# Performance work log

Hardware: AMD Instinct MI355X
Metric: run time of the kernel (lower is better)

## Reference

```python
import jax, jax.numpy as jnp
import numpy as np

B, H, G, EPG = 32768, 4096, 16, 16
E = G * EPG  # 256 total experts
STD = 0.02


def setup_inputs() -> dict:
    key = jax.random.key(0)
    k1, k2, k3 = jax.random.split(key, 3)
    hidden_states = jax.random.normal(k1, (B, H), dtype=jnp.float32)
    group_w = STD * jax.random.normal(k2, (G, H), dtype=jnp.float32)   # group_router.weight
    expert_w = STD * jax.random.normal(k3, (G, EPG, H), dtype=jnp.float32)  # stacked expert_routers[g].weight
    return {"hidden_states": hidden_states, "group_w": group_w, "expert_w": expert_w}


def reference(hidden_states, group_w, expert_w):
    b, h = hidden_states.shape
    g, epg, _ = expert_w.shape
    e = g * epg

    # Level 1: group routing (argmax of softmax == argmax of logits)
    group_logits = hidden_states @ group_w.T                      # [B, G]
    selected_groups = jnp.argmax(group_logits, axis=-1)           # [B]

    # Level 2: expert logits for every group, then gather the selected group's block.
    # (Math identical to per-token loop computing only the selected group's router.)
    logits_all = jnp.einsum('bh,geh->bge', hidden_states, expert_w)  # [B, G, EPG]
    sel_logits = jnp.take_along_axis(
        logits_all, selected_groups[:, None, None], axis=1)[:, 0, :]  # [B, EPG]

    expert_probs = jax.nn.softmax(sel_logits, axis=-1)            # [B, EPG]
    local_idx = jnp.argmax(expert_probs, axis=-1)                 # [B]
    selected_experts = selected_groups * epg + local_idx          # [B]
    expert_weights = jnp.take_along_axis(expert_probs, local_idx[:, None], axis=1)[:, 0]  # [B]

    # Scatter the selected group's logits into the global [B, E] tensor (rest zero).
    rows = jnp.arange(b)[:, None]                                 # [B, 1]
    cols = selected_groups[:, None] * epg + jnp.arange(epg)[None, :]  # [B, EPG]
    all_expert_logits = jnp.zeros((b, e), dtype=hidden_states.dtype).at[rows, cols].set(sel_logits)

    return all_expert_logits, selected_experts[:, None], expert_weights[:, None]
```

## Files before the change

### kernel.cpp

```cpp
#include <hip/hip_runtime.h>


constexpr int Btok = 32768;
constexpr int Hdim = 4096;
constexpr int Gn   = 16;
constexpr int EPGn = 16;
constexpr int En   = 256;
constexpr int Hq   = Hdim / 4;
constexpr int TILE = 1024;

__global__ __launch_bounds__(256) void k_group(
    const float* __restrict__ hidden, const float* __restrict__ gw,
    unsigned char* __restrict__ gsel)
{
  const int lane = threadIdx.x & 63;
  const int wq = __builtin_amdgcn_readfirstlane((int)(threadIdx.x >> 6));
  const int token = blockIdx.x * 64 + lane;
  const float* hrow  = hidden + (size_t)token * Hdim + wq * Hq;
  const float* wbase = gw + wq * Hq;

  float acc[Gn];
#pragma unroll
  for (int g = 0; g < Gn; ++g) acc[g] = 0.f;

#pragma unroll 2
  for (int j = 0; j < Hq; j += 4) {
    const float4 h4 = *reinterpret_cast<const float4*>(hrow + j);
#pragma unroll
    for (int g = 0; g < Gn; ++g) {
      const float* wg = wbase + g * Hdim + j;
      acc[g] += h4.x * wg[0] + h4.y * wg[1] + h4.z * wg[2] + h4.w * wg[3];
    }
  }

  __shared__ float part[4][64][Gn + 1];
#pragma unroll
  for (int g = 0; g < Gn; ++g) part[wq][lane][g] = acc[g];
  __syncthreads();

  if (wq == 0) {
    float best = -3.4e38f; int bi = 0;
#pragma unroll
    for (int g = 0; g < Gn; ++g) {
      float v = part[0][lane][g] + part[1][lane][g]
              + part[2][lane][g] + part[3][lane][g];
      if (v > best) { best = v; bi = g; }
    }
    gsel[token] = (unsigned char)bi;
  }
}

__global__ __launch_bounds__(256) void k_expert(
    const float* __restrict__ hidden, const float* __restrict__ ew,
    const unsigned char* __restrict__ gsel,
    float* __restrict__ out0,
    float* __restrict__ out1,
    float* __restrict__ out2)
{
  const int g = blockIdx.x;
  const int tbase = blockIdx.y * TILE;

  __shared__ int   list[TILE];
  __shared__ int   cnt;
  __shared__ float part[4][64][EPGn + 1];
  __shared__ float lrow[64][EPGn + 1];

  if (threadIdx.x == 0) cnt = 0;
  __syncthreads();
  for (int i = threadIdx.x; i < TILE; i += 256) {
    if ((int)gsel[tbase + i] == g) {
      int p = atomicAdd(&cnt, 1);
      list[p] = tbase + i;
    }
  }
  __syncthreads();
  const int n = cnt;

  const int lane = threadIdx.x & 63;
  const int wq = __builtin_amdgcn_readfirstlane((int)(threadIdx.x >> 6));
  const float* wbase = ew + ((size_t)g * EPGn) * Hdim + wq * Hq;

  for (int s0 = 0; s0 < n; s0 += 64) {
    const int ns = min(64, n - s0);
    const int token = list[s0 + ((lane < ns) ? lane : 0)];
    const float* hrow = hidden + (size_t)token * Hdim + wq * Hq;

    float acc[EPGn];
#pragma unroll
    for (int e = 0; e < EPGn; ++e) acc[e] = 0.f;

#pragma unroll 2
    for (int j = 0; j < Hq; j += 4) {
      const float4 h4 = *reinterpret_cast<const float4*>(hrow + j);
#pragma unroll
      for (int e = 0; e < EPGn; ++e) {
        const float* we = wbase + e * Hdim + j;
        acc[e] += h4.x * we[0] + h4.y * we[1] + h4.z * we[2] + h4.w * we[3];
      }
    }

#pragma unroll
    for (int e = 0; e < EPGn; ++e) part[wq][lane][e] = acc[e];
    __syncthreads();

    if (wq == 0 && lane < ns) {
      float l[EPGn];
      float m = -3.4e38f;
#pragma unroll
      for (int e = 0; e < EPGn; ++e) {
        l[e] = part[0][lane][e] + part[1][lane][e]
             + part[2][lane][e] + part[3][lane][e];
        m = fmaxf(m, l[e]);
      }
      float sum = 0.f;
#pragma unroll
      for (int e = 0; e < EPGn; ++e) sum += expf(l[e] - m);
      int bi = 0; float best = l[0];
#pragma unroll
      for (int e = 1; e < EPGn; ++e) { if (l[e] > best) { best = l[e]; bi = e; } }
      const int tok = list[s0 + lane];
      out1[tok] = (float)(g * EPGn + bi);
      out2[tok] = 1.f / sum;
#pragma unroll
      for (int e = 0; e < EPGn; ++e) lrow[lane][e] = l[e];
    }
    __syncthreads();

    const int r = threadIdx.x >> 2;
    const int p = threadIdx.x & 3;
    if (r < ns) {
      const int tok = list[s0 + r];
      float* row = out0 + (size_t)tok * En;
#pragma unroll
      for (int i = 0; i < 16; ++i) {
        float4 v;
        if (i == g) {
          v.x = lrow[r][p * 4 + 0];
          v.y = lrow[r][p * 4 + 1];
          v.z = lrow[r][p * 4 + 2];
          v.w = lrow[r][p * 4 + 3];
        } else {
          v.x = 0.f; v.y = 0.f; v.z = 0.f; v.w = 0.f;
        }
        *reinterpret_cast<float4*>(row + i * 16 + p * 4) = v;
      }
    }
    __syncthreads();
  }
}

extern "C" void kernel_launch(void* const* d_in, const int* in_sizes, int n_in,
                              void* d_out, int out_size, void* d_ws, size_t ws_size,
                              hipStream_t stream) {
  const float* hidden = (const float*)d_in[0];
  const float* gw     = (const float*)d_in[1];
  const float* ew     = (const float*)d_in[2];
  float* out0 = (float*)d_out;
  unsigned char* gsel = (unsigned char*)d_ws;

  k_group<<<Btok / 64, 256, 0, stream>>>(hidden, gw, gsel);

  float* out1 = out0 + (size_t)Btok * En;
  float* out2 = out1 + Btok;
  k_expert<<<dim3(Gn, Btok / TILE), 256, 0, stream>>>(
      hidden, ew, gsel, out0, out1, out2);
}
```

Measured before the change: 1.270 ms.

## Split hidden dim across 16 waves and parallelize reductions with shuffles

Both kernels move from 256-thread to 1024-thread blocks. The hidden dimension is now split across 16 wavefronts instead of 4, so each wave does a quarter of the dot-product work and occupancy rises. The partial sums are reduced in two LDS stages. Softmax, argmax and group-argmax then run in parallel across 16 lanes per token with xor shuffles, replacing a single wave that looped serially, and each lane writes one 16-wide slice of the output row. The change also uses the fast __expf, picks the lowest index on ties, and sets a launch bound of (1024, 8) that may squeeze register allocation.

```diff
diff --git a/kernel.cpp b/kernel.cpp
--- a/kernel.cpp
+++ b/kernel.cpp
@@ -6,25 +6,26 @@
 constexpr int Gn   = 16;
 constexpr int EPGn = 16;
 constexpr int En   = 256;
-constexpr int Hq   = Hdim / 4;
+constexpr int WV   = 16;
+constexpr int Hs   = Hdim / WV;
 constexpr int TILE = 1024;
 
-__global__ __launch_bounds__(256) void k_group(
+__global__ __launch_bounds__(1024, 8) void k_group(
     const float* __restrict__ hidden, const float* __restrict__ gw,
     unsigned char* __restrict__ gsel)
 {
   const int lane = threadIdx.x & 63;
   const int wq = __builtin_amdgcn_readfirstlane((int)(threadIdx.x >> 6));
   const int token = blockIdx.x * 64 + lane;
-  const float* hrow  = hidden + (size_t)token * Hdim + wq * Hq;
-  const float* wbase = gw + wq * Hq;
+  const float* hrow  = hidden + (size_t)token * Hdim + wq * Hs;
+  const float* wbase = gw + wq * Hs;
 
   float acc[Gn];
 #pragma unroll
   for (int g = 0; g < Gn; ++g) acc[g] = 0.f;
 
 #pragma unroll 2
-  for (int j = 0; j < Hq; j += 4) {
+  for (int j = 0; j < Hs; j += 4) {
     const float4 h4 = *reinterpret_cast<const float4*>(hrow + j);
 #pragma unroll
     for (int g = 0; g < Gn; ++g) {
@@ -33,24 +34,35 @@
     }
   }
 
-  __shared__ float part[4][64][Gn + 1];
+  __shared__ float part[8][64][Gn + 1];
+  if (wq >= 8) {
 #pragma unroll
-  for (int g = 0; g < Gn; ++g) part[wq][lane][g] = acc[g];
+    for (int g = 0; g < Gn; ++g) part[wq - 8][lane][g] = acc[g];
+  }
+  __syncthreads();
+  if (wq < 8) {
+#pragma unroll
+    for (int g = 0; g < Gn; ++g) part[wq][lane][g] += acc[g];
+  }
   __syncthreads();
 
-  if (wq == 0) {
-    float best = -3.4e38f; int bi = 0;
+  const int tok = threadIdx.x >> 4;
+  const int g   = threadIdx.x & 15;
+  float v = 0.f;
 #pragma unroll
-    for (int g = 0; g < Gn; ++g) {
-      float v = part[0][lane][g] + part[1][lane][g]
-              + part[2][lane][g] + part[3][lane][g];
-      if (v > best) { best = v; bi = g; }
-    }
-    gsel[token] = (unsigned char)bi;
+  for (int s = 0; s < 8; ++s) v += part[s][tok][g];
+
+  int bi = g;
+#pragma unroll
+  for (int off = 8; off; off >>= 1) {
+    float v2 = __shfl_xor(v, off);
+    int   i2 = __shfl_xor(bi, off);
+    if (v2 > v || (v2 == v && i2 < bi)) { v = v2; bi = i2; }
   }
+  if (g == 0) gsel[blockIdx.x * 64 + tok] = (unsigned char)bi;
 }
 
-__global__ __launch_bounds__(256) void k_expert(
+__global__ __launch_bounds__(1024, 8) void k_expert(
     const float* __restrict__ hidden, const float* __restrict__ ew,
     const unsigned char* __restrict__ gsel,
     float* __restrict__ out0,
@@ -62,12 +74,12 @@
 
   __shared__ int   list[TILE];
   __shared__ int   cnt;
-  __shared__ float part[4][64][EPGn + 1];
+  __shared__ float part[8][64][EPGn + 1];
   __shared__ float lrow[64][EPGn + 1];
 
   if (threadIdx.x == 0) cnt = 0;
   __syncthreads();
-  for (int i = threadIdx.x; i < TILE; i += 256) {
+  for (int i = threadIdx.x; i < TILE; i += 1024) {
     if ((int)gsel[tbase + i] == g) {
       int p = atomicAdd(&cnt, 1);
       list[p] = tbase + i;
@@ -78,19 +90,19 @@
 
   const int lane = threadIdx.x & 63;
   const int wq = __builtin_amdgcn_readfirstlane((int)(threadIdx.x >> 6));
-  const float* wbase = ew + ((size_t)g * EPGn) * Hdim + wq * Hq;
+  const float* wbase = ew + ((size_t)g * EPGn) * Hdim + wq * Hs;
 
   for (int s0 = 0; s0 < n; s0 += 64) {
     const int ns = min(64, n - s0);
     const int token = list[s0 + ((lane < ns) ? lane : 0)];
-    const float* hrow = hidden + (size_t)token * Hdim + wq * Hq;
+    const float* hrow = hidden + (size_t)token * Hdim + wq * Hs;
 
     float acc[EPGn];
 #pragma unroll
     for (int e = 0; e < EPGn; ++e) acc[e] = 0.f;
 
 #pragma unroll 2
-    for (int j = 0; j < Hq; j += 4) {
+    for (int j = 0; j < Hs; j += 4) {
       const float4 h4 = *reinterpret_cast<const float4*>(hrow + j);
 #pragma unroll
       for (int e = 0; e < EPGn; ++e) {
@@ -99,50 +111,64 @@
       }
     }
 
+    if (wq >= 8) {
 #pragma unroll
-    for (int e = 0; e < EPGn; ++e) part[wq][lane][e] = acc[e];
+      for (int e = 0; e < EPGn; ++e) part[wq - 8][lane][e] = acc[e];
+    }
     __syncthreads();
-
-    if (wq == 0 && lane < ns) {
-      float l[EPGn];
-      float m = -3.4e38f;
+    if (wq < 8) {
 #pragma unroll
-      for (int e = 0; e < EPGn; ++e) {
-        l[e] = part[0][lane][e] + part[1][lane][e]
-             + part[2][lane][e] + part[3][lane][e];
-        m = fmaxf(m, l[e]);
-      }
-      float sum = 0.f;
-#pragma unroll
-      for (int e = 0; e < EPGn; ++e) sum += expf(l[e] - m);
-      int bi = 0; float best = l[0];
-#pragma unroll
-      for (int e = 1; e < EPGn; ++e) { if (l[e] > best) { best = l[e]; bi = e; } }
-      const int tok = list[s0 + lane];
-      out1[tok] = (float)(g * EPGn + bi);
-      out2[tok] = 1.f / sum;
-#pragma unroll
-      for (int e = 0; e < EPGn; ++e) lrow[lane][e] = l[e];
+      for (int e = 0; e < EPGn; ++e) part[wq][lane][e] += acc[e];
     }
     __syncthreads();
 
-    const int r = threadIdx.x >> 2;
-    const int p = threadIdx.x & 3;
+    const int tk = threadIdx.x >> 4;
+    const int e  = threadIdx.x & 15;
+    float l = 0.f;
+#pragma unroll
+    for (int s = 0; s < 8; ++s) l += part[s][tk][e];
+    lrow[tk][e] = l;
+
+    float m = l;
+#pragma unroll
+    for (int off = 8; off; off >>= 1) m = fmaxf(m, __shfl_xor(m, off));
+    float sum = __expf(l - m);
+#pragma unroll
+    for (int off = 8; off; off >>= 1) sum += __shfl_xor(sum, off);
+
+    float v = l; int bi = e;
+#pragma unroll
+    for (int off = 8; off; off >>= 1) {
+      float v2 = __shfl_xor(v, off);
+      int   i2 = __shfl_xor(bi, off);
+      if (v2 > v || (v2 == v && i2 < bi)) { v = v2; bi = i2; }
+    }
+    if (e == 0 && tk < ns) {
+      const int tok = list[s0 + tk];
+      out1[tok] = (float)(g * EPGn + bi);
+      out2[tok] = 1.f / sum;
+    }
+
+    const int r = tk;
+    const int p = e;
     if (r < ns) {
       const int tok = list[s0 + r];
-      float* row = out0 + (size_t)tok * En;
+      float* row = out0 + (size_t)tok * En + p * 16;
+      if (p == g) {
 #pragma unroll
-      for (int i = 0; i < 16; ++i) {
-        float4 v;
-        if (i == g) {
-          v.x = lrow[r][p * 4 + 0];
-          v.y = lrow[r][p * 4 + 1];
-          v.z = lrow[r][p * 4 + 2];
-          v.w = lrow[r][p * 4 + 3];
-        } else {
-          v.x = 0.f; v.y = 0.f; v.z = 0.f; v.w = 0.f;
+        for (int q = 0; q < 4; ++q) {
+          float4 v4;
+          v4.x = lrow[r][q * 4 + 0];
+          v4.y = lrow[r][q * 4 + 1];
+          v4.z = lrow[r][q * 4 + 2];
+          v4.w = lrow[r][q * 4 + 3];
+          *reinterpret_cast<float4*>(row + q * 4) = v4;
         }
-        *reinterpret_cast<float4*>(row + i * 16 + p * 4) = v;
+      } else {
+        const float4 z = {0.f, 0.f, 0.f, 0.f};
+#pragma unroll
+        for (int q = 0; q < 4; ++q)
+          *reinterpret_cast<float4*>(row + q * 4) = z;
       }
     }
     __syncthreads();
@@ -158,10 +184,10 @@
   float* out0 = (float*)d_out;
   unsigned char* gsel = (unsigned char*)d_ws;
 
-  k_group<<<Btok / 64, 256, 0, stream>>>(hidden, gw, gsel);
+  k_group<<<Btok / 64, 1024, 0, stream>>>(hidden, gw, gsel);
 
   float* out1 = out0 + (size_t)Btok * En;
   float* out2 = out1 + Btok;
-  k_expert<<<dim3(Gn, Btok / TILE), 256, 0, stream>>>(
+  k_expert<<<dim3(Gn, Btok / TILE), 1024, 0, stream>>>(
       hidden, ew, gsel, out0, out1, out2);
 }
```

New measurement: 1.187 ms. 1.07x faster.
